# Performance work log

Measured on AMD Instinct MI355X. Metric: run time of the kernel, lower is better.

The kernel has to match this reference:

```python
import jax, jax.numpy as jnp
import numpy as np

D, H, V, T_MAX, L = 1024, 16, 32000, 1024, 8
B, T = 2, 1024
EPS = 1e-5


def setup_inputs() -> dict:
    key = jax.random.key(0)
    ks = jax.random.split(key, 12)
    s = 0.02
    w = lambda k, shape: (jax.random.normal(k, shape, jnp.float32) * s)
    return {
        "tokens": jax.random.randint(ks[0], (B, T), 0, V),
        "emb": w(ks[1], (V, D)),
        "pos_emb": w(ks[2], (T_MAX, D)),
        "ln1_s": jnp.ones((L, D)), "ln1_b": jnp.zeros((L, D)),
        "Wq": w(ks[3], (L, D, D)), "bq": jnp.zeros((L, D)),
        "Wk": w(ks[4], (L, D, D)), "bk": jnp.zeros((L, D)),
        "Wv": w(ks[5], (L, D, D)), "bv": jnp.zeros((L, D)),
        "Wo": w(ks[6], (L, D, D)), "bo": jnp.zeros((L, D)),
        "ln2_s": jnp.ones((L, D)), "ln2_b": jnp.zeros((L, D)),
        "W1": w(ks[7], (L, D, 4 * D)), "b1": jnp.zeros((L, 4 * D)),
        "W2": w(ks[8], (L, 4 * D, D)), "b2": jnp.zeros((L, D)),
        "lnf_s": jnp.ones((D,)), "lnf_b": jnp.zeros((D,)),
        "Wl": w(ks[9], (D, V)), "bl": jnp.zeros((V,)),
    }


def _layernorm(x, scale, bias):
    m = jnp.mean(x, -1, keepdims=True)
    v = jnp.mean(jnp.square(x - m), -1, keepdims=True)
    return (x - m) * jax.lax.rsqrt(v + EPS) * scale + bias


def _gpt(tokens, emb, pos_emb, ln1_s, ln1_b, Wq, bq, Wk, bk, Wv, bv, Wo, bo,
         ln2_s, ln2_b, W1, b1, W2, b2, lnf_s, lnf_b, Wl, bl):
    b_, t_ = tokens.shape
    dh = D // H
    x = emb[tokens] + pos_emb[:t_]  # (B,T,D)
    causal = jnp.tril(jnp.ones((t_, t_), bool))
    for i in range(L):
        h = _layernorm(x, ln1_s[i], ln1_b[i])
        q = (h @ Wq[i] + bq[i]).reshape(b_, t_, H, dh).transpose(0, 2, 1, 3)
        k = (h @ Wk[i] + bk[i]).reshape(b_, t_, H, dh).transpose(0, 2, 1, 3)
        v = (h @ Wv[i] + bv[i]).reshape(b_, t_, H, dh).transpose(0, 2, 1, 3)
        scores = jnp.einsum('bhqd,bhkd->bhqk', q, k) / np.sqrt(dh).astype(np.float32)
        scores = jnp.where(causal, scores, -jnp.inf)
        attn = jax.nn.softmax(scores, axis=-1)
        y = jnp.einsum('bhqk,bhkd->bhqd', attn, v)
        y = y.transpose(0, 2, 1, 3).reshape(b_, t_, D)
        x = x + (y @ Wo[i] + bo[i])
        h = _layernorm(x, ln2_s[i], ln2_b[i])
        # torch nn.GELU default = exact erf gelu
        x = x + (jax.nn.gelu(h @ W1[i] + b1[i], approximate=False) @ W2[i] + b2[i])
    x = _layernorm(x, lnf_s, lnf_b)
    return x @ Wl + bl  # (B,T,V) logits


def reference(tokens, emb, pos_emb, ln1_s, ln1_b, Wq, bq, Wk, bk, Wv, bv, Wo, bo,
              ln2_s, ln2_b, W1, b1, W2, b2, lnf_s, lnf_b, Wl, bl):
    return _gpt(tokens, emb, pos_emb, ln1_s, ln1_b, Wq, bq, Wk, bk, Wv, bv, Wo, bo,
                ln2_s, ln2_b, W1, b1, W2, b2, lnf_s, lnf_b, Wl, bl)
```

## Files before the change

### kernel.cpp

```cpp
#include <hip/hip_runtime.h>
#include <hip/hip_bf16.h>
#include <math.h>

constexpr int kD = 1024;
constexpr int kH = 16;
constexpr int kDH = 64;
constexpr int kV = 32000;
constexpr int kL = 8;
constexpr int kB = 2;
constexpr int kT = 1024;
constexpr int kRows = kB * kT;
constexpr float kEPS = 1e-5f;

typedef __attribute__((ext_vector_type(8))) short short8v;
typedef __attribute__((ext_vector_type(4))) float f32x4;

__device__ __forceinline__ uint32_t pk2(float a, float b) {
    union { float f; uint32_t u; } x, y;
    x.f = a; y.f = b;
    uint32_t lo = (x.u + 0x7FFFu + ((x.u >> 16) & 1)) >> 16;
    uint32_t hi = (y.u + 0x7FFFu + ((y.u >> 16) & 1)) >> 16;
    return lo | (hi << 16);
}
__device__ __forceinline__ unsigned short bf1(float a) {
    union { float f; uint32_t u; } x; x.f = a;
    return (unsigned short)((x.u + 0x7FFFu + ((x.u >> 16) & 1)) >> 16);
}

__device__ __forceinline__ int swz(int idx, int kg) {
    return idx * 4 + (kg ^ ((idx ^ (idx >> 2)) & 3));
}

__global__ __launch_bounds__(256) void embed_kernel(
    const int* __restrict__ tokens, const float* __restrict__ emb,
    const float* __restrict__ pos, float* __restrict__ x)
{
    int row = blockIdx.x;
    int t = row % kT;
    int tok = tokens[row];
    const float4* e = (const float4*)(emb + (size_t)tok * kD);
    const float4* p = (const float4*)(pos + (size_t)t * kD);
    float4* o = (float4*)(x + (size_t)row * kD);
    int i = threadIdx.x;
    float4 a = e[i], b4 = p[i];
    o[i] = make_float4(a.x + b4.x, a.y + b4.y, a.z + b4.z, a.w + b4.w);
}

__global__ __launch_bounds__(256) void ln_kernel(
    const float* __restrict__ x, const float* __restrict__ sc,
    const float* __restrict__ bi, float* __restrict__ out)
{
    int row = blockIdx.x;
    int tid = threadIdx.x;
    float4 v4 = ((const float4*)(x + (size_t)row * kD))[tid];

    __shared__ float red1[4];
    __shared__ float red2[4];

    float s = v4.x + v4.y + v4.z + v4.w;
    #pragma unroll
    for (int off = 32; off > 0; off >>= 1) s += __shfl_down(s, off);
    if ((tid & 63) == 0) red1[tid >> 6] = s;
    __syncthreads();
    float mean = (red1[0] + red1[1] + red1[2] + red1[3]) * (1.0f / kD);

    float dx = v4.x - mean, dy = v4.y - mean, dz = v4.z - mean, dw = v4.w - mean;
    float vs = dx * dx + dy * dy + dz * dz + dw * dw;
    #pragma unroll
    for (int off = 32; off > 0; off >>= 1) vs += __shfl_down(vs, off);
    if ((tid & 63) == 0) red2[tid >> 6] = vs;
    __syncthreads();
    float var = (red2[0] + red2[1] + red2[2] + red2[3]) * (1.0f / kD);
    float inv = rsqrtf(var + kEPS);

    float4 s4 = ((const float4*)sc)[tid];
    float4 b4 = ((const float4*)bi)[tid];
    float4 o;
    o.x = dx * inv * s4.x + b4.x;
    o.y = dy * inv * s4.y + b4.y;
    o.z = dz * inv * s4.z + b4.z;
    o.w = dw * inv * s4.w + b4.w;
    ((float4*)(out + (size_t)row * kD))[tid] = o;
}

template<int BM, int BN, int EPI>
__device__ __forceinline__ void mgemm_body(
    const float* __restrict__ A, const float* __restrict__ W,
    const float* __restrict__ bias, const float* __restrict__ res,
    float* __restrict__ C, int N, int K, int bm, int bn)
{
    constexpr int KSTEP = 32;
    constexpr int FM = (BM / 2) / 16;
    constexpr int FN = (BN / 2) / 16;
    constexpr int A_PER = (BM * 4) / 256;
    constexpr int KPT = BN / 32;
    constexpr int NMASK = BN / 4 - 1;
    constexpr int KQSH = (BN == 128) ? 5 : 4;

    __shared__ uint4 smem[BM * 4 + BN * 4];
    char* sA = (char*)smem;
    char* sB = (char*)(smem + BM * 4);

    int tid = threadIdx.x;
    int lane = tid & 63;
    int wv = tid >> 6;
    int wr = wv >> 1, wc = wv & 1;
    int fr = lane & 15;
    int kg = lane >> 4;

    int n4 = tid & NMASK;
    int kq = tid >> KQSH;
    int kbase = kq * KPT;

    f32x4 acc[FM][FN] = {};
    float4 pa[A_PER][2];
    float4 pb[KPT];

    auto loadA = [&](int k0) {
        #pragma unroll
        for (int s = 0; s < A_PER; ++s) {
            int slot = tid * A_PER + s;
            int row = slot >> 2, k8 = slot & 3;
            const float* p = A + (size_t)(bm + row) * K + k0 + k8 * 8;
            pa[s][0] = *(const float4*)p;
            pa[s][1] = *(const float4*)(p + 4);
        }
    };
    auto loadB = [&](int k0) {
        #pragma unroll
        for (int i = 0; i < KPT; ++i)
            pb[i] = *(const float4*)(W + (size_t)(k0 + kbase + i) * N + bn + n4 * 4);
    };
    auto writeA = [&]() {
        #pragma unroll
        for (int s = 0; s < A_PER; ++s) {
            int slot = tid * A_PER + s;
            int row = slot >> 2, k8 = slot & 3;
            uint4 w;
            w.x = pk2(pa[s][0].x, pa[s][0].y);
            w.y = pk2(pa[s][0].z, pa[s][0].w);
            w.z = pk2(pa[s][1].x, pa[s][1].y);
            w.w = pk2(pa[s][1].z, pa[s][1].w);
            *(uint4*)(sA + swz(row, k8) * 16) = w;
        }
    };
    auto writeB = [&]() {
        int kgc = kbase >> 3;
        int kb8 = (kbase & 7) * 2;
        #pragma unroll
        for (int j = 0; j < 4; ++j) {
            int col = n4 * 4 + j;
            char* dst = sB + swz(col, kgc) * 16 + kb8;
            if constexpr (KPT == 4) {
                uint2 w;
                w.x = pk2((&pb[0].x)[j], (&pb[1].x)[j]);
                w.y = pk2((&pb[2].x)[j], (&pb[3].x)[j]);
                *(uint2*)dst = w;
            } else {
                *(uint32_t*)dst = pk2((&pb[0].x)[j], (&pb[1].x)[j]);
            }
        }
    };
    auto compute = [&]() {
        short8v af[FM], bf[FN];
        #pragma unroll
        for (int mi = 0; mi < FM; ++mi) {
            int row = wr * (BM / 2) + mi * 16 + fr;
            af[mi] = *(const short8v*)(sA + swz(row, kg) * 16);
        }
        #pragma unroll
        for (int nj = 0; nj < FN; ++nj) {
            int col = wc * (BN / 2) + nj * 16 + fr;
            bf[nj] = *(const short8v*)(sB + swz(col, kg) * 16);
        }
        #pragma unroll
        for (int mi = 0; mi < FM; ++mi)
            #pragma unroll
            for (int nj = 0; nj < FN; ++nj)
                acc[mi][nj] = __builtin_amdgcn_mfma_f32_16x16x32_bf16(
                    af[mi], bf[nj], acc[mi][nj], 0, 0, 0);
    };

    loadA(0); loadB(0);
    writeA(); writeB();
    __syncthreads();

    for (int k0 = 0; k0 < K; k0 += KSTEP) {
        bool more = (k0 + KSTEP) < K;
        if (more) { loadA(k0 + KSTEP); loadB(k0 + KSTEP); }
        compute();
        __syncthreads();
        if (more) {
            writeA(); writeB();
            __syncthreads();
        }
    }

    #pragma unroll
    for (int mi = 0; mi < FM; ++mi) {
        #pragma unroll
        for (int nj = 0; nj < FN; ++nj) {
            int col = bn + wc * (BN / 2) + nj * 16 + fr;
            float bia = bias[col];
            #pragma unroll
            for (int r = 0; r < 4; ++r) {
                int row = bm + wr * (BM / 2) + mi * 16 + kg * 4 + r;
                float o = acc[mi][nj][r] + bia;
                if (EPI == 1) o += res[(size_t)row * N + col];
                if (EPI == 2) o = 0.5f * o * (1.0f + erff(o * 0.70710678118f));
                C[(size_t)row * N + col] = o;
            }
        }
    }
}

template<int BM, int BN, int EPI>
__global__ __launch_bounds__(256) void mgemm_kernel(
    const float* __restrict__ A, const float* __restrict__ W,
    const float* __restrict__ bias, const float* __restrict__ res,
    float* __restrict__ C, int N, int K)
{
    mgemm_body<BM, BN, EPI>(A, W, bias, res, C, N, K,
                            blockIdx.y * BM, blockIdx.x * BN);
}

__global__ __launch_bounds__(256) void mgemm_qkv_kernel(
    const float* __restrict__ A,
    const float* __restrict__ Wq, const float* __restrict__ bq, float* __restrict__ qo,
    const float* __restrict__ Wk, const float* __restrict__ bk, float* __restrict__ ko,
    const float* __restrict__ Wv, const float* __restrict__ bv, float* __restrict__ vo)
{
    const float* W = (blockIdx.z == 0) ? Wq : (blockIdx.z == 1) ? Wk : Wv;
    const float* b = (blockIdx.z == 0) ? bq : (blockIdx.z == 1) ? bk : bv;
    float* C       = (blockIdx.z == 0) ? qo : (blockIdx.z == 1) ? ko : vo;
    mgemm_body<128, 64, 0>(A, W, b, nullptr, C, kD, kD,
                           blockIdx.y * 128, blockIdx.x * 64);
}

__global__ __launch_bounds__(256) void fattn_kernel(
    const float* __restrict__ q, const float* __restrict__ k,
    const float* __restrict__ v, float* __restrict__ y)
{
    int qt = (int)(gridDim.x - 1) - (int)blockIdx.x;
    int h = blockIdx.y;
    int b = blockIdx.z;
    int q0 = qt * 64;

    __shared__ __align__(16) char sQ[8192];
    __shared__ __align__(16) char sK[8192];
    __shared__ __align__(16) char sVT[8192];
    __shared__ __align__(16) char sP[4][2048];

    int tid = threadIdx.x;
    int lane = tid & 63;
    int w = tid >> 6;
    int fr = lane & 15;
    int g4 = lane >> 4;

    const float* qbase = q + (size_t)(b * kT) * kD + h * kDH;
    const float* kbase = k + (size_t)(b * kT) * kD + h * kDH;
    const float* vbase = v + (size_t)(b * kT) * kD + h * kDH;

    int srow = tid >> 2;
    int c4 = tid & 3;

    {
        const float* src = qbase + (size_t)(q0 + srow) * kD + c4 * 16;
        float4 f0 = ((const float4*)src)[0];
        float4 f1 = ((const float4*)src)[1];
        float4 f2 = ((const float4*)src)[2];
        float4 f3 = ((const float4*)src)[3];
        const float s8 = 0.125f;
        uint4 w0, w1;
        w0.x = pk2(f0.x * s8, f0.y * s8); w0.y = pk2(f0.z * s8, f0.w * s8);
        w0.z = pk2(f1.x * s8, f1.y * s8); w0.w = pk2(f1.z * s8, f1.w * s8);
        w1.x = pk2(f2.x * s8, f2.y * s8); w1.y = pk2(f2.z * s8, f2.w * s8);
        w1.z = pk2(f3.x * s8, f3.y * s8); w1.w = pk2(f3.z * s8, f3.w * s8);
        *(uint4*)(sQ + srow * 128 + (((c4 * 2)     ^ (srow & 7)) * 16)) = w0;
        *(uint4*)(sQ + srow * 128 + (((c4 * 2 + 1) ^ (srow & 7)) * 16)) = w1;
    }
    __syncthreads();

    short8v aq[2];
    {
        int row = w * 16 + fr;
        aq[0] = *(const short8v*)(sQ + row * 128 + (((g4)     ^ (fr & 7)) * 16));
        aq[1] = *(const short8v*)(sQ + row * 128 + (((4 + g4) ^ (fr & 7)) * 16));
    }

    f32x4 accO[4] = {};
    float mrow[4], lrow[4];
    #pragma unroll
    for (int r = 0; r < 4; ++r) { mrow[r] = -INFINITY; lrow[r] = 0.0f; }

    int ntiles = qt + 1;
    for (int t = 0; t < ntiles; ++t) {
        int k0 = t * 64;
        __syncthreads();
        {
            const float* src = kbase + (size_t)(k0 + srow) * kD + c4 * 16;
            float4 f0 = ((const float4*)src)[0];
            float4 f1 = ((const float4*)src)[1];
            float4 f2 = ((const float4*)src)[2];
            float4 f3 = ((const float4*)src)[3];
            uint4 w0, w1;
            w0.x = pk2(f0.x, f0.y); w0.y = pk2(f0.z, f0.w);
            w0.z = pk2(f1.x, f1.y); w0.w = pk2(f1.z, f1.w);
            w1.x = pk2(f2.x, f2.y); w1.y = pk2(f2.z, f2.w);
            w1.z = pk2(f3.x, f3.y); w1.w = pk2(f3.z, f3.w);
            *(uint4*)(sK + srow * 128 + (((c4 * 2)     ^ (srow & 7)) * 16)) = w0;
            *(uint4*)(sK + srow * 128 + (((c4 * 2 + 1) ^ (srow & 7)) * 16)) = w1;
        }
        {
            const float* src = vbase + (size_t)(k0 + srow) * kD + c4 * 16;
            int kg = srow >> 3;
            int kb2 = (srow & 7) * 2;
            #pragma unroll
            for (int j = 0; j < 4; ++j) {
                float4 f = ((const float4*)src)[j];
                int dbase = c4 * 16 + j * 4;
                *(unsigned short*)(sVT + (dbase + 0) * 128 + ((kg ^ ((dbase + 0) & 7)) * 16) + kb2) = bf1(f.x);
                *(unsigned short*)(sVT + (dbase + 1) * 128 + ((kg ^ ((dbase + 1) & 7)) * 16) + kb2) = bf1(f.y);
                *(unsigned short*)(sVT + (dbase + 2) * 128 + ((kg ^ ((dbase + 2) & 7)) * 16) + kb2) = bf1(f.z);
                *(unsigned short*)(sVT + (dbase + 3) * 128 + ((kg ^ ((dbase + 3) & 7)) * 16) + kb2) = bf1(f.w);
            }
        }
        __syncthreads();

        f32x4 s[4];
        #pragma unroll
        for (int nj = 0; nj < 4; ++nj) { s[nj][0] = 0; s[nj][1] = 0; s[nj][2] = 0; s[nj][3] = 0; }
        #pragma unroll
        for (int nj = 0; nj < 4; ++nj) {
            int krow = nj * 16 + fr;
            short8v bk0 = *(const short8v*)(sK + krow * 128 + (((g4)     ^ (fr & 7)) * 16));
            short8v bk1 = *(const short8v*)(sK + krow * 128 + (((4 + g4) ^ (fr & 7)) * 16));
            s[nj] = __builtin_amdgcn_mfma_f32_16x16x32_bf16(aq[0], bk0, s[nj], 0, 0, 0);
            s[nj] = __builtin_amdgcn_mfma_f32_16x16x32_bf16(aq[1], bk1, s[nj], 0, 0, 0);
        }

        if (t == qt) {
            #pragma unroll
            for (int nj = 0; nj < 4; ++nj)
                #pragma unroll
                for (int r = 0; r < 4; ++r) {
                    int qq = w * 16 + g4 * 4 + r;
                    int kk = nj * 16 + fr;
                    if (kk > qq) s[nj][r] = -1e30f;
                }
        }

        float tm[4];
        #pragma unroll
        for (int r = 0; r < 4; ++r)
            tm[r] = fmaxf(fmaxf(s[0][r], s[1][r]), fmaxf(s[2][r], s[3][r]));
        #pragma unroll
        for (int mk = 1; mk <= 8; mk <<= 1)
            #pragma unroll
            for (int r = 0; r < 4; ++r)
                tm[r] = fmaxf(tm[r], __shfl_xor(tm[r], mk));

        float scl[4];
        #pragma unroll
        for (int r = 0; r < 4; ++r) {
            float mnew = fmaxf(mrow[r], tm[r]);
            scl[r] = __expf(mrow[r] - mnew);
            mrow[r] = mnew;
        }
        float ps[4][4];
        float psum[4];
        #pragma unroll
        for (int r = 0; r < 4; ++r) {
            ps[0][r] = __expf(s[0][r] - mrow[r]);
            ps[1][r] = __expf(s[1][r] - mrow[r]);
            ps[2][r] = __expf(s[2][r] - mrow[r]);
            ps[3][r] = __expf(s[3][r] - mrow[r]);
            psum[r] = ps[0][r] + ps[1][r] + ps[2][r] + ps[3][r];
        }
        #pragma unroll
        for (int mk = 1; mk <= 8; mk <<= 1)
            #pragma unroll
            for (int r = 0; r < 4; ++r)
                psum[r] += __shfl_xor(psum[r], mk);
        #pragma unroll
        for (int r = 0; r < 4; ++r)
            lrow[r] = lrow[r] * scl[r] + psum[r];
        #pragma unroll
        for (int nj = 0; nj < 4; ++nj)
            #pragma unroll
            for (int r = 0; r < 4; ++r)
                accO[nj][r] *= scl[r];

        #pragma unroll
        for (int nj = 0; nj < 4; ++nj) {
            int kk = nj * 16 + fr;
            int kg = nj * 2 + (fr >> 3);
            #pragma unroll
            for (int r = 0; r < 4; ++r) {
                int qq = g4 * 4 + r;
                *(unsigned short*)(sP[w] + qq * 128 + ((kg ^ (qq & 7)) * 16) + (fr & 7) * 2) = bf1(ps[nj][r]);
            }
        }
        #pragma unroll
        for (int ks = 0; ks < 2; ++ks) {
            short8v ap = *(const short8v*)(sP[w] + fr * 128 + (((ks * 4 + g4) ^ (fr & 7)) * 16));
            #pragma unroll
            for (int nj = 0; nj < 4; ++nj) {
                int drow = nj * 16 + fr;
                short8v bv_ = *(const short8v*)(sVT + drow * 128 + (((ks * 4 + g4) ^ (fr & 7)) * 16));
                accO[nj] = __builtin_amdgcn_mfma_f32_16x16x32_bf16(ap, bv_, accO[nj], 0, 0, 0);
            }
        }
    }

    float invl[4];
    #pragma unroll
    for (int r = 0; r < 4; ++r) invl[r] = 1.0f / lrow[r];
    #pragma unroll
    for (int nj = 0; nj < 4; ++nj) {
        #pragma unroll
        for (int r = 0; r < 4; ++r) {
            int qg = q0 + w * 16 + g4 * 4 + r;
            int d = nj * 16 + fr;
            y[(size_t)(b * kT + qg) * kD + h * kDH + d] = accO[nj][r] * invl[r];
        }
    }
}

extern "C" void kernel_launch(void* const* d_in, const int* in_sizes, int n_in,
                              void* d_out, int out_size, void* d_ws, size_t ws_size,
                              hipStream_t stream)
{
    const int*   tokens = (const int*)  d_in[0];
    const float* emb    = (const float*)d_in[1];
    const float* pos    = (const float*)d_in[2];
    const float* ln1_s  = (const float*)d_in[3];
    const float* ln1_b  = (const float*)d_in[4];
    const float* Wq     = (const float*)d_in[5];
    const float* bq     = (const float*)d_in[6];
    const float* Wk     = (const float*)d_in[7];
    const float* bk     = (const float*)d_in[8];
    const float* Wv     = (const float*)d_in[9];
    const float* bv     = (const float*)d_in[10];
    const float* Wo     = (const float*)d_in[11];
    const float* bo     = (const float*)d_in[12];
    const float* ln2_s  = (const float*)d_in[13];
    const float* ln2_b  = (const float*)d_in[14];
    const float* W1     = (const float*)d_in[15];
    const float* b1     = (const float*)d_in[16];
    const float* W2     = (const float*)d_in[17];
    const float* b2     = (const float*)d_in[18];
    const float* lnf_s  = (const float*)d_in[19];
    const float* lnf_b  = (const float*)d_in[20];
    const float* Wl     = (const float*)d_in[21];
    const float* bl     = (const float*)d_in[22];
    float* out = (float*)d_out;

    size_t BTD = (size_t)kRows * kD;
    float* ws  = (float*)d_ws;
    float* x   = ws;
    float* h   = x + BTD;
    float* qb  = h + BTD;
    float* kb  = qb + BTD;
    float* vb  = kb + BTD;
    float* mid = qb;

    embed_kernel<<<kRows, 256, 0, stream>>>(tokens, emb, pos, x);

    dim3 gQkv(kD / 64, kRows / 128, 3);
    dim3 gProj(kD / 64, kRows / 128);
    dim3 gFfn1(4 * kD / 128, kRows / 128);
    dim3 gLogit(kV / 128, kRows / 128);
    dim3 gAttn(kT / 64, kH, kB);

    for (int i = 0; i < kL; ++i) {
        size_t oD  = (size_t)i * kD;
        size_t oDD = (size_t)i * kD * kD;
        size_t oD4 = (size_t)i * 4 * kD;
        size_t oDD4 = (size_t)i * kD * 4 * kD;

        ln_kernel<<<kRows, 256, 0, stream>>>(x, ln1_s + oD, ln1_b + oD, h);

        mgemm_qkv_kernel<<<gQkv, 256, 0, stream>>>(h,
            Wq + oDD, bq + oD, qb,
            Wk + oDD, bk + oD, kb,
            Wv + oDD, bv + oD, vb);

        fattn_kernel<<<gAttn, 256, 0, stream>>>(qb, kb, vb, h);

        mgemm_kernel<128, 64, 1><<<gProj, 256, 0, stream>>>(h, Wo + oDD, bo + oD, x, x, kD, kD);

        ln_kernel<<<kRows, 256, 0, stream>>>(x, ln2_s + oD, ln2_b + oD, h);

        mgemm_kernel<128, 128, 2><<<gFfn1, 256, 0, stream>>>(h, W1 + oDD4, b1 + oD4, nullptr, mid, 4 * kD, kD);
        mgemm_kernel<128, 64, 1><<<gProj, 256, 0, stream>>>(mid, W2 + oDD4, b2 + oD, x, x, kD, 4 * kD);
    }

    ln_kernel<<<kRows, 256, 0, stream>>>(x, lnf_s, lnf_b, h);
    mgemm_kernel<128, 128, 0><<<gLogit, 256, 0, stream>>>(h, Wl, bl, nullptr, out, kV, kD);
}
```

Before: 3.742 ms.

## Keep activations in bf16 and pre-transpose weights to bf16 each call

Adds a weight conversion kernel that transposes and casts every fp32 weight matrix to bf16 (K-contiguous) at the start of each call. LayerNorm, the QKV projection, attention and FFN1 now emit bf16 activations, and the GEMMs load bf16 A/B tiles straight into shared memory without per-tile packing. The aim is to halve activation traffic and drop the conversion work from the GEMM inner loops. In exchange, every call pays for converting roughly 170M weight elements and needs a much larger workspace, with a fallback to the old fp32 path when the workspace is too small.

```diff
diff --git a/kernel.cpp b/kernel.cpp
--- a/kernel.cpp
+++ b/kernel.cpp
@@ -12,6 +12,7 @@
 constexpr int kRows = kB * kT;
 constexpr float kEPS = 1e-5f;
 
+typedef unsigned short u16;
 typedef __attribute__((ext_vector_type(8))) short short8v;
 typedef __attribute__((ext_vector_type(4))) float f32x4;
 
@@ -22,9 +23,9 @@
     uint32_t hi = (y.u + 0x7FFFu + ((y.u >> 16) & 1)) >> 16;
     return lo | (hi << 16);
 }
-__device__ __forceinline__ unsigned short bf1(float a) {
+__device__ __forceinline__ u16 bf1(float a) {
     union { float f; uint32_t u; } x; x.f = a;
-    return (unsigned short)((x.u + 0x7FFFu + ((x.u >> 16) & 1)) >> 16);
+    return (u16)((x.u + 0x7FFFu + ((x.u >> 16) & 1)) >> 16);
 }
 
 __device__ __forceinline__ int swz(int idx, int kg) {
@@ -46,9 +47,38 @@
     o[i] = make_float4(a.x + b4.x, a.y + b4.y, a.z + b4.z, a.w + b4.w);
 }
 
+__global__ __launch_bounds__(256) void wconv_kernel(
+    const float* __restrict__ inp, u16* __restrict__ outp, int K, int N)
+{
+    __shared__ float tile[64][65];
+    int k0 = blockIdx.x * 64;
+    int n0 = blockIdx.y * 64;
+    size_t zin = (size_t)blockIdx.z * (size_t)K * N;
+    size_t zout = (size_t)blockIdx.z * (size_t)N * K;
+    int tr = threadIdx.x >> 4;
+    int tc = (threadIdx.x & 15) * 4;
+    #pragma unroll
+    for (int i = 0; i < 4; ++i) {
+        int r = tr + i * 16;
+        float4 f = *(const float4*)(inp + zin + (size_t)(k0 + r) * N + n0 + tc);
+        tile[r][tc + 0] = f.x; tile[r][tc + 1] = f.y;
+        tile[r][tc + 2] = f.z; tile[r][tc + 3] = f.w;
+    }
+    __syncthreads();
+    #pragma unroll
+    for (int i = 0; i < 4; ++i) {
+        int n = tr + i * 16;
+        uint2 w;
+        w.x = pk2(tile[tc + 0][n], tile[tc + 1][n]);
+        w.y = pk2(tile[tc + 2][n], tile[tc + 3][n]);
+        *(uint2*)(outp + zout + (size_t)(n0 + n) * K + k0 + tc) = w;
+    }
+}
+
+template<bool OUTB>
 __global__ __launch_bounds__(256) void ln_kernel(
     const float* __restrict__ x, const float* __restrict__ sc,
-    const float* __restrict__ bi, float* __restrict__ out)
+    const float* __restrict__ bi, void* __restrict__ outv)
 {
     int row = blockIdx.x;
     int tid = threadIdx.x;
@@ -75,27 +105,27 @@
 
     float4 s4 = ((const float4*)sc)[tid];
     float4 b4 = ((const float4*)bi)[tid];
-    float4 o;
-    o.x = dx * inv * s4.x + b4.x;
-    o.y = dy * inv * s4.y + b4.y;
-    o.z = dz * inv * s4.z + b4.z;
-    o.w = dw * inv * s4.w + b4.w;
-    ((float4*)(out + (size_t)row * kD))[tid] = o;
-}
-
-template<int BM, int BN, int EPI>
+    float ox = dx * inv * s4.x + b4.x;
+    float oy = dy * inv * s4.y + b4.y;
+    float oz = dz * inv * s4.z + b4.z;
+    float ow = dw * inv * s4.w + b4.w;
+    if constexpr (OUTB) {
+        uint2 w; w.x = pk2(ox, oy); w.y = pk2(oz, ow);
+        ((uint2*)((u16*)outv + (size_t)row * kD))[tid] = w;
+    } else {
+        ((float4*)((float*)outv + (size_t)row * kD))[tid] = make_float4(ox, oy, oz, ow);
+    }
+}
+
+template<int BM, int BN, int EPI, bool INB, bool OUTB>
 __device__ __forceinline__ void mgemm_body(
-    const float* __restrict__ A, const float* __restrict__ W,
+    const void* __restrict__ Av, const void* __restrict__ Wv_,
     const float* __restrict__ bias, const float* __restrict__ res,
-    float* __restrict__ C, int N, int K, int bm, int bn)
+    void* __restrict__ Cv, int N, int K, int bm, int bn)
 {
     constexpr int KSTEP = 32;
     constexpr int FM = (BM / 2) / 16;
     constexpr int FN = (BN / 2) / 16;
-    constexpr int A_PER = (BM * 4) / 256;
-    constexpr int KPT = BN / 32;
-    constexpr int NMASK = BN / 4 - 1;
-    constexpr int KQSH = (BN == 128) ? 5 : 4;
 
     __shared__ uint4 smem[BM * 4 + BN * 4];
     char* sA = (char*)smem;
@@ -108,59 +138,8 @@
     int fr = lane & 15;
     int kg = lane >> 4;
 
-    int n4 = tid & NMASK;
-    int kq = tid >> KQSH;
-    int kbase = kq * KPT;
-
     f32x4 acc[FM][FN] = {};
-    float4 pa[A_PER][2];
-    float4 pb[KPT];
-
-    auto loadA = [&](int k0) {
-        #pragma unroll
-        for (int s = 0; s < A_PER; ++s) {
-            int slot = tid * A_PER + s;
-            int row = slot >> 2, k8 = slot & 3;
-            const float* p = A + (size_t)(bm + row) * K + k0 + k8 * 8;
-            pa[s][0] = *(const float4*)p;
-            pa[s][1] = *(const float4*)(p + 4);
-        }
-    };
-    auto loadB = [&](int k0) {
-        #pragma unroll
-        for (int i = 0; i < KPT; ++i)
-            pb[i] = *(const float4*)(W + (size_t)(k0 + kbase + i) * N + bn + n4 * 4);
-    };
-    auto writeA = [&]() {
-        #pragma unroll
-        for (int s = 0; s < A_PER; ++s) {
-            int slot = tid * A_PER + s;
-            int row = slot >> 2, k8 = slot & 3;
-            uint4 w;
-            w.x = pk2(pa[s][0].x, pa[s][0].y);
-            w.y = pk2(pa[s][0].z, pa[s][0].w);
-            w.z = pk2(pa[s][1].x, pa[s][1].y);
-            w.w = pk2(pa[s][1].z, pa[s][1].w);
-            *(uint4*)(sA + swz(row, k8) * 16) = w;
-        }
-    };
-    auto writeB = [&]() {
-        int kgc = kbase >> 3;
-        int kb8 = (kbase & 7) * 2;
-        #pragma unroll
-        for (int j = 0; j < 4; ++j) {
-            int col = n4 * 4 + j;
-            char* dst = sB + swz(col, kgc) * 16 + kb8;
-            if constexpr (KPT == 4) {
-                uint2 w;
-                w.x = pk2((&pb[0].x)[j], (&pb[1].x)[j]);
-                w.y = pk2((&pb[2].x)[j], (&pb[3].x)[j]);
-                *(uint2*)dst = w;
-            } else {
-                *(uint32_t*)dst = pk2((&pb[0].x)[j], (&pb[1].x)[j]);
-            }
-        }
-    };
+
     auto compute = [&]() {
         short8v af[FM], bf[FN];
         #pragma unroll
@@ -181,18 +160,121 @@
                     af[mi], bf[nj], acc[mi][nj], 0, 0, 0);
     };
 
-    loadA(0); loadB(0);
-    writeA(); writeB();
-    __syncthreads();
-
-    for (int k0 = 0; k0 < K; k0 += KSTEP) {
-        bool more = (k0 + KSTEP) < K;
-        if (more) { loadA(k0 + KSTEP); loadB(k0 + KSTEP); }
-        compute();
+    if constexpr (INB) {
+        const u16* A = (const u16*)Av;
+        const u16* Wt = (const u16*)Wv_;
+        constexpr int A_PER = (BM * 4) / 256;
+        constexpr int B_PER = (BN * 4) / 256;
+        uint4 pa[A_PER], pb[B_PER];
+        auto loadAB = [&](int k0) {
+            #pragma unroll
+            for (int s = 0; s < A_PER; ++s) {
+                int slot = tid * A_PER + s;
+                int row = slot >> 2, k8 = slot & 3;
+                pa[s] = *(const uint4*)(A + (size_t)(bm + row) * K + k0 + k8 * 8);
+            }
+            #pragma unroll
+            for (int s = 0; s < B_PER; ++s) {
+                int slot = tid * B_PER + s;
+                int col = slot >> 2, kc = slot & 3;
+                pb[s] = *(const uint4*)(Wt + (size_t)(bn + col) * K + k0 + kc * 8);
+            }
+        };
+        auto writeAB = [&]() {
+            #pragma unroll
+            for (int s = 0; s < A_PER; ++s) {
+                int slot = tid * A_PER + s;
+                int row = slot >> 2, k8 = slot & 3;
+                *(uint4*)(sA + swz(row, k8) * 16) = pa[s];
+            }
+            #pragma unroll
+            for (int s = 0; s < B_PER; ++s) {
+                int slot = tid * B_PER + s;
+                int col = slot >> 2, kc = slot & 3;
+                *(uint4*)(sB + swz(col, kc) * 16) = pb[s];
+            }
+        };
+        loadAB(0); writeAB();
         __syncthreads();
-        if (more) {
-            writeA(); writeB();
+        for (int k0 = 0; k0 < K; k0 += KSTEP) {
+            bool more = (k0 + KSTEP) < K;
+            if (more) loadAB(k0 + KSTEP);
+            compute();
             __syncthreads();
+            if (more) {
+                writeAB();
+                __syncthreads();
+            }
+        }
+    } else {
+        const float* A = (const float*)Av;
+        const float* W = (const float*)Wv_;
+        constexpr int A_PER = (BM * 4) / 256;
+        constexpr int KPT = BN / 32;
+        constexpr int NMASK = BN / 4 - 1;
+        constexpr int KQSH = (BN == 128) ? 5 : 4;
+        int n4 = tid & NMASK;
+        int kq = tid >> KQSH;
+        int kbase = kq * KPT;
+        float4 pa[A_PER][2];
+        float4 pb[KPT];
+        auto loadA = [&](int k0) {
+            #pragma unroll
+            for (int s = 0; s < A_PER; ++s) {
+                int slot = tid * A_PER + s;
+                int row = slot >> 2, k8 = slot & 3;
+                const float* p = A + (size_t)(bm + row) * K + k0 + k8 * 8;
+                pa[s][0] = *(const float4*)p;
+                pa[s][1] = *(const float4*)(p + 4);
+            }
+        };
+        auto loadB = [&](int k0) {
+            #pragma unroll
+            for (int i = 0; i < KPT; ++i)
+                pb[i] = *(const float4*)(W + (size_t)(k0 + kbase + i) * N + bn + n4 * 4);
+        };
+        auto writeA = [&]() {
+            #pragma unroll
+            for (int s = 0; s < A_PER; ++s) {
+                int slot = tid * A_PER + s;
+                int row = slot >> 2, k8 = slot & 3;
+                uint4 w;
+                w.x = pk2(pa[s][0].x, pa[s][0].y);
+                w.y = pk2(pa[s][0].z, pa[s][0].w);
+                w.z = pk2(pa[s][1].x, pa[s][1].y);
+                w.w = pk2(pa[s][1].z, pa[s][1].w);
+                *(uint4*)(sA + swz(row, k8) * 16) = w;
+            }
+        };
+        auto writeB = [&]() {
+            int kgc = kbase >> 3;
+            int kb8 = (kbase & 7) * 2;
+            #pragma unroll
+            for (int j = 0; j < 4; ++j) {
+                int col = n4 * 4 + j;
+                char* dst = sB + swz(col, kgc) * 16 + kb8;
+                if constexpr (KPT == 4) {
+                    uint2 w;
+                    w.x = pk2((&pb[0].x)[j], (&pb[1].x)[j]);
+                    w.y = pk2((&pb[2].x)[j], (&pb[3].x)[j]);
+                    *(uint2*)dst = w;
+                } else {
+                    *(uint32_t*)dst = pk2((&pb[0].x)[j], (&pb[1].x)[j]);
+                }
+            }
+        };
+        loadA(0); loadB(0);
+        writeA(); writeB();
+        __syncthreads();
+        for (int k0 = 0; k0 < K; k0 += KSTEP) {
+            bool more = (k0 + KSTEP) < K;
+            if (more) { loadA(k0 + KSTEP); loadB(k0 + KSTEP); }
+            compute();
+            __syncthreads();
+            if (more) {
+                writeA(); writeB();
+                __syncthreads();
+            }
         }
     }
 
@@ -208,38 +290,43 @@
                 float o = acc[mi][nj][r] + bia;
                 if (EPI == 1) o += res[(size_t)row * N + col];
                 if (EPI == 2) o = 0.5f * o * (1.0f + erff(o * 0.70710678118f));
-                C[(size_t)row * N + col] = o;
-            }
-        }
-    }
-}
-
-template<int BM, int BN, int EPI>
+                if constexpr (OUTB)
+                    ((u16*)Cv)[(size_t)row * N + col] = bf1(o);
+                else
+                    ((float*)Cv)[(size_t)row * N + col] = o;
+            }
+        }
+    }
+}
+
+template<int BM, int BN, int EPI, bool INB, bool OUTB>
 __global__ __launch_bounds__(256) void mgemm_kernel(
-    const float* __restrict__ A, const float* __restrict__ W,
+    const void* __restrict__ A, const void* __restrict__ W,
     const float* __restrict__ bias, const float* __restrict__ res,
-    float* __restrict__ C, int N, int K)
-{
-    mgemm_body<BM, BN, EPI>(A, W, bias, res, C, N, K,
-                            blockIdx.y * BM, blockIdx.x * BN);
-}
-
-__global__ __launch_bounds__(256) void mgemm_qkv_kernel(
-    const float* __restrict__ A,
-    const float* __restrict__ Wq, const float* __restrict__ bq, float* __restrict__ qo,
-    const float* __restrict__ Wk, const float* __restrict__ bk, float* __restrict__ ko,
-    const float* __restrict__ Wv, const float* __restrict__ bv, float* __restrict__ vo)
-{
-    const float* W = (blockIdx.z == 0) ? Wq : (blockIdx.z == 1) ? Wk : Wv;
-    const float* b = (blockIdx.z == 0) ? bq : (blockIdx.z == 1) ? bk : bv;
-    float* C       = (blockIdx.z == 0) ? qo : (blockIdx.z == 1) ? ko : vo;
-    mgemm_body<128, 64, 0>(A, W, b, nullptr, C, kD, kD,
-                           blockIdx.y * 128, blockIdx.x * 64);
-}
-
+    void* __restrict__ C, int N, int K)
+{
+    mgemm_body<BM, BN, EPI, INB, OUTB>(A, W, bias, res, C, N, K,
+                                       blockIdx.x * BM, blockIdx.y * BN);
+}
+
+template<bool FAST>
+__global__ __launch_bounds__(256) void qkv_kernel(
+    const void* __restrict__ A,
+    const void* __restrict__ W0, const float* __restrict__ b0, void* __restrict__ C0,
+    const void* __restrict__ W1, const float* __restrict__ b1, void* __restrict__ C1,
+    const void* __restrict__ W2, const float* __restrict__ b2, void* __restrict__ C2)
+{
+    const void* W = (blockIdx.z == 0) ? W0 : (blockIdx.z == 1) ? W1 : W2;
+    const float* b = (blockIdx.z == 0) ? b0 : (blockIdx.z == 1) ? b1 : b2;
+    void* C        = (blockIdx.z == 0) ? C0 : (blockIdx.z == 1) ? C1 : C2;
+    mgemm_body<128, 64, 0, FAST, FAST>(A, W, b, nullptr, C, kD, kD,
+                                       blockIdx.x * 128, blockIdx.y * 64);
+}
+
+template<bool B16>
 __global__ __launch_bounds__(256) void fattn_kernel(
-    const float* __restrict__ q, const float* __restrict__ k,
-    const float* __restrict__ v, float* __restrict__ y)
+    const void* __restrict__ qv, const void* __restrict__ kv,
+    const void* __restrict__ vv, void* __restrict__ yv)
 {
     int qt = (int)(gridDim.x - 1) - (int)blockIdx.x;
     int h = blockIdx.y;
@@ -257,15 +344,17 @@
     int fr = lane & 15;
     int g4 = lane >> 4;
 
-    const float* qbase = q + (size_t)(b * kT) * kD + h * kDH;
-    const float* kbase = k + (size_t)(b * kT) * kD + h * kDH;
-    const float* vbase = v + (size_t)(b * kT) * kD + h * kDH;
-
     int srow = tid >> 2;
     int c4 = tid & 3;
 
-    {
-        const float* src = qbase + (size_t)(q0 + srow) * kD + c4 * 16;
+    if constexpr (B16) {
+        const u16* src = (const u16*)qv + (size_t)(b * kT + q0 + srow) * kD + h * kDH + c4 * 16;
+        uint4 w0 = ((const uint4*)src)[0];
+        uint4 w1 = ((const uint4*)src)[1];
+        *(uint4*)(sQ + srow * 128 + (((c4 * 2)     ^ (srow & 7)) * 16)) = w0;
+        *(uint4*)(sQ + srow * 128 + (((c4 * 2 + 1) ^ (srow & 7)) * 16)) = w1;
+    } else {
+        const float* src = (const float*)qv + (size_t)(b * kT + q0 + srow) * kD + h * kDH + c4 * 16;
         float4 f0 = ((const float4*)src)[0];
         float4 f1 = ((const float4*)src)[1];
         float4 f2 = ((const float4*)src)[2];
@@ -297,8 +386,14 @@
     for (int t = 0; t < ntiles; ++t) {
         int k0 = t * 64;
         __syncthreads();
-        {
-            const float* src = kbase + (size_t)(k0 + srow) * kD + c4 * 16;
+        if constexpr (B16) {
+            const u16* src = (const u16*)kv + (size_t)(b * kT + k0 + srow) * kD + h * kDH + c4 * 16;
+            uint4 w0 = ((const uint4*)src)[0];
+            uint4 w1 = ((const uint4*)src)[1];
+            *(uint4*)(sK + srow * 128 + (((c4 * 2)     ^ (srow & 7)) * 16)) = w0;
+            *(uint4*)(sK + srow * 128 + (((c4 * 2 + 1) ^ (srow & 7)) * 16)) = w1;
+        } else {
+            const float* src = (const float*)kv + (size_t)(b * kT + k0 + srow) * kD + h * kDH + c4 * 16;
             float4 f0 = ((const float4*)src)[0];
             float4 f1 = ((const float4*)src)[1];
             float4 f2 = ((const float4*)src)[2];
@@ -312,17 +407,29 @@
             *(uint4*)(sK + srow * 128 + (((c4 * 2 + 1) ^ (srow & 7)) * 16)) = w1;
         }
         {
-            const float* src = vbase + (size_t)(k0 + srow) * kD + c4 * 16;
             int kg = srow >> 3;
             int kb2 = (srow & 7) * 2;
-            #pragma unroll
-            for (int j = 0; j < 4; ++j) {
-                float4 f = ((const float4*)src)[j];
-                int dbase = c4 * 16 + j * 4;
-                *(unsigned short*)(sVT + (dbase + 0) * 128 + ((kg ^ ((dbase + 0) & 7)) * 16) + kb2) = bf1(f.x);
-                *(unsigned short*)(sVT + (dbase + 1) * 128 + ((kg ^ ((dbase + 1) & 7)) * 16) + kb2) = bf1(f.y);
-                *(unsigned short*)(sVT + (dbase + 2) * 128 + ((kg ^ ((dbase + 2) & 7)) * 16) + kb2) = bf1(f.z);
-                *(unsigned short*)(sVT + (dbase + 3) * 128 + ((kg ^ ((dbase + 3) & 7)) * 16) + kb2) = bf1(f.w);
+            if constexpr (B16) {
+                const u16* src = (const u16*)vv + (size_t)(b * kT + k0 + srow) * kD + h * kDH + c4 * 16;
+                u16 vals[16];
+                *(uint4*)(vals) = ((const uint4*)src)[0];
+                *(uint4*)(vals + 8) = ((const uint4*)src)[1];
+                #pragma unroll
+                for (int j = 0; j < 16; ++j) {
+                    int d = c4 * 16 + j;
+                    *(u16*)(sVT + d * 128 + ((kg ^ (d & 7)) * 16) + kb2) = vals[j];
+                }
+            } else {
+                const float* src = (const float*)vv + (size_t)(b * kT + k0 + srow) * kD + h * kDH + c4 * 16;
+                #pragma unroll
+                for (int j = 0; j < 4; ++j) {
+                    float4 f = ((const float4*)src)[j];
+                    int dbase = c4 * 16 + j * 4;
+                    *(u16*)(sVT + (dbase + 0) * 128 + ((kg ^ ((dbase + 0) & 7)) * 16) + kb2) = bf1(f.x);
+                    *(u16*)(sVT + (dbase + 1) * 128 + ((kg ^ ((dbase + 1) & 7)) * 16) + kb2) = bf1(f.y);
+                    *(u16*)(sVT + (dbase + 2) * 128 + ((kg ^ ((dbase + 2) & 7)) * 16) + kb2) = bf1(f.z);
+                    *(u16*)(sVT + (dbase + 3) * 128 + ((kg ^ ((dbase + 3) & 7)) * 16) + kb2) = bf1(f.w);
+                }
             }
         }
         __syncthreads();
@@ -337,6 +444,12 @@
             short8v bk1 = *(const short8v*)(sK + krow * 128 + (((4 + g4) ^ (fr & 7)) * 16));
             s[nj] = __builtin_amdgcn_mfma_f32_16x16x32_bf16(aq[0], bk0, s[nj], 0, 0, 0);
             s[nj] = __builtin_amdgcn_mfma_f32_16x16x32_bf16(aq[1], bk1, s[nj], 0, 0, 0);
+        }
+        if constexpr (B16) {
+            #pragma unroll
+            for (int nj = 0; nj < 4; ++nj)
+                #pragma unroll
+                for (int r = 0; r < 4; ++r) s[nj][r] *= 0.125f;
         }
 
         if (t == qt) {
@@ -393,12 +506,11 @@
 
         #pragma unroll
         for (int nj = 0; nj < 4; ++nj) {
-            int kk = nj * 16 + fr;
             int kg = nj * 2 + (fr >> 3);
             #pragma unroll
             for (int r = 0; r < 4; ++r) {
                 int qq = g4 * 4 + r;
-                *(unsigned short*)(sP[w] + qq * 128 + ((kg ^ (qq & 7)) * 16) + (fr & 7) * 2) = bf1(ps[nj][r]);
+                *(u16*)(sP[w] + qq * 128 + ((kg ^ (qq & 7)) * 16) + (fr & 7) * 2) = bf1(ps[nj][r]);
             }
         }
         #pragma unroll
@@ -422,7 +534,11 @@
         for (int r = 0; r < 4; ++r) {
             int qg = q0 + w * 16 + g4 * 4 + r;
             int d = nj * 16 + fr;
-            y[(size_t)(b * kT + qg) * kD + h * kDH + d] = accO[nj][r] * invl[r];
+            float o = accO[nj][r] * invl[r];
+            if constexpr (B16)
+                ((u16*)yv)[(size_t)(b * kT + qg) * kD + h * kDH + d] = bf1(o);
+            else
+                ((float*)yv)[(size_t)(b * kT + qg) * kD + h * kDH + d] = o;
         }
     }
 }
@@ -457,45 +573,102 @@
     float* out = (float*)d_out;
 
     size_t BTD = (size_t)kRows * kD;
-    float* ws  = (float*)d_ws;
-    float* x   = ws;
-    float* h   = x + BTD;
-    float* qb  = h + BTD;
-    float* kb  = qb + BTD;
-    float* vb  = kb + BTD;
-    float* mid = qb;
-
-    embed_kernel<<<kRows, 256, 0, stream>>>(tokens, emb, pos, x);
-
-    dim3 gQkv(kD / 64, kRows / 128, 3);
-    dim3 gProj(kD / 64, kRows / 128);
-    dim3 gFfn1(4 * kD / 128, kRows / 128);
-    dim3 gLogit(kV / 128, kRows / 128);
+    size_t DD  = (size_t)kD * kD;
+
+    float* x    = (float*)d_ws;
+    u16* h16    = (u16*)(x + BTD);
+    u16* qb16   = h16 + BTD;
+    u16* kb16   = qb16 + BTD;
+    u16* vb16   = kb16 + BTD;
+    u16* mid16  = vb16 + BTD;
+    u16* wqt    = mid16 + 4 * BTD;
+    u16* wkt    = wqt + (size_t)kL * DD;
+    u16* wvt    = wkt + (size_t)kL * DD;
+    u16* wot    = wvt + (size_t)kL * DD;
+    u16* w1t    = wot + (size_t)kL * DD;
+    u16* w2t    = w1t + (size_t)kL * 4 * DD;
+    u16* wlt    = w2t + (size_t)kL * 4 * DD;
+    u16* wend   = wlt + (size_t)kV * kD;
+    size_t need = (size_t)((char*)wend - (char*)d_ws);
+    bool fast = ws_size >= need;
+
     dim3 gAttn(kT / 64, kH, kB);
 
-    for (int i = 0; i < kL; ++i) {
-        size_t oD  = (size_t)i * kD;
-        size_t oDD = (size_t)i * kD * kD;
-        size_t oD4 = (size_t)i * 4 * kD;
-        size_t oDD4 = (size_t)i * kD * 4 * kD;
-
-        ln_kernel<<<kRows, 256, 0, stream>>>(x, ln1_s + oD, ln1_b + oD, h);
-
-        mgemm_qkv_kernel<<<gQkv, 256, 0, stream>>>(h,
-            Wq + oDD, bq + oD, qb,
-            Wk + oDD, bk + oD, kb,
-            Wv + oDD, bv + oD, vb);
-
-        fattn_kernel<<<gAttn, 256, 0, stream>>>(qb, kb, vb, h);
-
-        mgemm_kernel<128, 64, 1><<<gProj, 256, 0, stream>>>(h, Wo + oDD, bo + oD, x, x, kD, kD);
-
-        ln_kernel<<<kRows, 256, 0, stream>>>(x, ln2_s + oD, ln2_b + oD, h);
-
-        mgemm_kernel<128, 128, 2><<<gFfn1, 256, 0, stream>>>(h, W1 + oDD4, b1 + oD4, nullptr, mid, 4 * kD, kD);
-        mgemm_kernel<128, 64, 1><<<gProj, 256, 0, stream>>>(mid, W2 + oDD4, b2 + oD, x, x, kD, 4 * kD);
-    }
-
-    ln_kernel<<<kRows, 256, 0, stream>>>(x, lnf_s, lnf_b, h);
-    mgemm_kernel<128, 128, 0><<<gLogit, 256, 0, stream>>>(h, Wl, bl, nullptr, out, kV, kD);
-}
+    if (fast) {
+        wconv_kernel<<<dim3(16, 16, kL), 256, 0, stream>>>(Wq, wqt, kD, kD);
+        wconv_kernel<<<dim3(16, 16, kL), 256, 0, stream>>>(Wk, wkt, kD, kD);
+        wconv_kernel<<<dim3(16, 16, kL), 256, 0, stream>>>(Wv, wvt, kD, kD);
+        wconv_kernel<<<dim3(16, 16, kL), 256, 0, stream>>>(Wo, wot, kD, kD);
+        wconv_kernel<<<dim3(16, 64, kL), 256, 0, stream>>>(W1, w1t, kD, 4 * kD);
+        wconv_kernel<<<dim3(64, 16, kL), 256, 0, stream>>>(W2, w2t, 4 * kD, kD);
+        wconv_kernel<<<dim3(16, 500, 1), 256, 0, stream>>>(Wl, wlt, kD, kV);
+
+        embed_kernel<<<kRows, 256, 0, stream>>>(tokens, emb, pos, x);
+
+        for (int i = 0; i < kL; ++i) {
+            size_t oD  = (size_t)i * kD;
+            size_t oD4 = (size_t)i * 4 * kD;
+
+            ln_kernel<true><<<kRows, 256, 0, stream>>>(x, ln1_s + oD, ln1_b + oD, h16);
+
+            qkv_kernel<true><<<dim3(16, 16, 3), 256, 0, stream>>>(h16,
+                wqt + i * DD, bq + oD, qb16,
+                wkt + i * DD, bk + oD, kb16,
+                wvt + i * DD, bv + oD, vb16);
+
+            fattn_kernel<true><<<gAttn, 256, 0, stream>>>(qb16, kb16, vb16, h16);
+
+            mgemm_kernel<128, 64, 1, true, false><<<dim3(16, 16), 256, 0, stream>>>(
+                h16, wot + i * DD, bo + oD, x, x, kD, kD);
+
+            ln_kernel<true><<<kRows, 256, 0, stream>>>(x, ln2_s + oD, ln2_b + oD, h16);
+
+            mgemm_kernel<128, 128, 2, true, true><<<dim3(16, 32), 256, 0, stream>>>(
+                h16, w1t + i * 4 * DD, b1 + oD4, nullptr, mid16, 4 * kD, kD);
+            mgemm_kernel<128, 64, 1, true, false><<<dim3(16, 16), 256, 0, stream>>>(
+                mid16, w2t + i * 4 * DD, b2 + oD, x, x, kD, 4 * kD);
+        }
+
+        ln_kernel<true><<<kRows, 256, 0, stream>>>(x, lnf_s, lnf_b, h16);
+        mgemm_kernel<128, 128, 0, true, false><<<dim3(16, 250), 256, 0, stream>>>(
+            h16, wlt, bl, nullptr, out, kV, kD);
+    } else {
+        float* h   = x + BTD;
+        float* qb  = h + BTD;
+        float* kb  = qb + BTD;
+        float* vb  = kb + BTD;
+        float* mid = qb;
+
+        embed_kernel<<<kRows, 256, 0, stream>>>(tokens, emb, pos, x);
+
+        for (int i = 0; i < kL; ++i) {
+            size_t oD  = (size_t)i * kD;
+            size_t oDD = (size_t)i * DD;
+            size_t oD4 = (size_t)i * 4 * kD;
+            size_t oDD4 = (size_t)i * 4 * DD;
+
+            ln_kernel<false><<<kRows, 256, 0, stream>>>(x, ln1_s + oD, ln1_b + oD, h);
+
+            qkv_kernel<false><<<dim3(16, 16, 3), 256, 0, stream>>>(h,
+                Wq + oDD, bq + oD, qb,
+                Wk + oDD, bk + oD, kb,
+                Wv + oDD, bv + oD, vb);
+
+            fattn_kernel<false><<<gAttn, 256, 0, stream>>>(qb, kb, vb, h);
+
+            mgemm_kernel<128, 64, 1, false, false><<<dim3(16, 16), 256, 0, stream>>>(
+                h, Wo + oDD, bo + oD, x, x, kD, kD);
+
+            ln_kernel<false><<<kRows, 256, 0, stream>>>(x, ln2_s + oD, ln2_b + oD, h);
+
+            mgemm_kernel<128, 128, 2, false, false><<<dim3(16, 32), 256, 0, stream>>>(
+                h, W1 + oDD4, b1 + oD4, nullptr, mid, 4 * kD, kD);
+            mgemm_kernel<128, 64, 1, false, false><<<dim3(16, 16), 256, 0, stream>>>(
+                mid, W2 + oDD4, b2 + oD, x, x, kD, 4 * kD);
+        }
+
+        ln_kernel<false><<<kRows, 256, 0, stream>>>(x, lnf_s, lnf_b, h);
+        mgemm_kernel<128, 128, 0, false, false><<<dim3(16, 250), 256, 0, stream>>>(
+            h, Wl, bl, nullptr, out, kV, kD);
+    }
+}
```

Result: slower. 3.948 ms (+5.5%).
